# Kernel tuning notes

Hardware: AMD Instinct MI355X
Metric: run time of the kernel (lower is better)

The kernel has to match this reference:

```python
import jax, jax.numpy as jnp
import numpy as np

B, Q, D, E, V, K = 128, 32, 512, 300, 50000, 21

def kernel_mus(n):
    mus = [1.0]
    if n == 1:
        return mus
    bin_size = 2.0 / (n - 1)
    mus.append(1 - bin_size / 2)
    for i in range(1, n - 1):
        mus.append(mus[i] - bin_size)
    return mus

def kernel_sigmas(n):
    if n == 1:
        return [0.001]
    return [0.001] + [0.1] * (n - 1)

MU = jnp.asarray(kernel_mus(K), dtype=jnp.float32)        # (K,)
SIGMA = jnp.asarray(kernel_sigmas(K), dtype=jnp.float32)  # (K,)

def setup_inputs() -> dict:
    key = jax.random.key(0)
    k1, k2, k3, k4, k5, k6, k7 = jax.random.split(key, 7)
    query_idx = jax.random.randint(k1, (B, Q), 0, V)
    doc_idx = jax.random.randint(k2, (B, D), 0, V)
    query_len = jax.random.randint(k3, (B,), 1, Q + 1)
    doc_len = jax.random.randint(k4, (B,), 1, D + 1)
    emb_table = jax.random.normal(k5, (V, E), dtype=jnp.float32) * 0.1
    dense_w = jax.random.normal(k6, (1, K), dtype=jnp.float32) * 0.1
    dense_b = jax.random.normal(k7, (1,), dtype=jnp.float32) * 0.1
    return {"query_idx": query_idx, "doc_idx": doc_idx,
            "query_len": query_len, "doc_len": doc_len,
            "emb_table": emb_table, "dense_w": dense_w, "dense_b": dense_b}

def _l2norm(x):
    # F.normalize(x, p=2, dim=2): x / max(||x||, 1e-12)
    n = jnp.sqrt(jnp.sum(x * x, axis=-1, keepdims=True))
    return x / jnp.maximum(n, 1e-12)

def reference(query_idx, doc_idx, query_len, doc_len, emb_table, dense_w, dense_b):
    q_embed = _l2norm(emb_table[query_idx])   # (B,Q,E)
    d_embed = _l2norm(emb_table[doc_idx])     # (B,D,E)
    mask_q = (jnp.arange(Q)[None, :] < query_len[:, None]).astype(jnp.float32)  # (B,Q)
    mask_d = (jnp.arange(D)[None, :] < doc_len[:, None]).astype(jnp.float32)    # (B,D)
    sim = jnp.einsum('bqe,bde->bqd', q_embed, d_embed)  # (B,Q,D)
    # Gaussian kernel pooling: (B,Q,D,K) broadcast
    diff = sim[..., None] - MU
    pooling = jnp.exp(-(diff * diff) / (2.0 * SIGMA * SIGMA)) * mask_d[:, None, :, None]
    pooling_sum = jnp.sum(pooling, axis=2)                      # (B,Q,K)
    log_pool = jnp.log(jnp.clip(pooling_sum, 1e-10)) * mask_q[..., None] * 0.01
    log_pooling_sum = jnp.sum(log_pool, axis=1)                 # (B,K)
    score = jnp.squeeze(log_pooling_sum @ dense_w.T + dense_b, axis=1)  # (B,)
    return (score, log_pooling_sum)
```

## Files before the change

### kernel.cpp

```cpp
#include <hip/hip_runtime.h>

#define Bn 128
#define Qn 32
#define Dn 512
#define En 300
#define Kn 21
#define NC 16
#define CH 32
#define NKT 10
#define LDE 40
#define TILE_SH (CH * LDE)
#define SIMLD 36
#define NTHR 256
#define QK (Qn * Kn)

typedef __attribute__((ext_vector_type(8))) short bf16x8;
typedef __attribute__((ext_vector_type(4))) float f32x4;

#define SMEM_BYTES 51456

__device__ __forceinline__ float dot4(float4 a, float4 b) {
    return a.x * b.x + a.y * b.y + a.z * b.z + a.w * b.w;
}

#define ISSUE(arr, tok)                                                        \
    _Pragma("unroll")                                                          \
    for (int j2 = 0; j2 < NKT; ++j2) {                                         \
        const int k = j2 * 32 + il * 4;                                        \
        float4 v = {0.f, 0.f, 0.f, 0.f};                                       \
        if (k <= 296 && (tok) >= 0)                                            \
            v = *(const float4*)(table + (size_t)(tok) * En + k);              \
        arr[j2] = v;                                                           \
    }

#define COMMIT(arr, dst)                                                       \
    {                                                                          \
        float ss = 0.f;                                                        \
        _Pragma("unroll")                                                      \
        for (int j2 = 0; j2 < NKT; ++j2) ss += dot4(arr[j2], arr[j2]);         \
        ss += __shfl_xor(ss, 1);                                               \
        ss += __shfl_xor(ss, 2);                                               \
        ss += __shfl_xor(ss, 4);                                               \
        const float inv = 1.0f / fmaxf(sqrtf(ss), 1e-12f);                     \
        _Pragma("unroll")                                                      \
        for (int j2 = 0; j2 < NKT; ++j2) {                                     \
            const unsigned ax = __float_as_uint(arr[j2].x * inv) + 0x8000u;    \
            const unsigned ay = __float_as_uint(arr[j2].y * inv) + 0x8000u;    \
            const unsigned az = __float_as_uint(arr[j2].z * inv) + 0x8000u;    \
            const unsigned aw = __float_as_uint(arr[j2].w * inv) + 0x8000u;    \
            uint2 p;                                                           \
            p.x = __builtin_amdgcn_perm(ay, ax, 0x07060302u);                  \
            p.y = __builtin_amdgcn_perm(aw, az, 0x07060302u);                  \
            *(uint2*)&(dst)[j2 * TILE_SH + row * LDE + il * 4] = p;            \
        }                                                                      \
    }

__global__ __launch_bounds__(NTHR, 3)
void knrm_main(const int* __restrict__ qidx, const int* __restrict__ didx,
               const int* __restrict__ dlen_arr, const float* __restrict__ table,
               float* __restrict__ partial)
{
    const int g = blockIdx.x;
    const int idx2 = (g & 7) * 256 + (g >> 3);
    const int b = idx2 >> 4;
    const int c = idx2 & 15;
    const int dlen = dlen_arr[b];
    if (c * CH >= dlen) return;

    const int t = threadIdx.x;

    __shared__ __align__(16) char smem[SMEM_BYTES];
    short* dbuf = (short*)smem;
    short* qbuf = (short*)(smem + 25600);
    float* sim  = (float*)(smem + 25600);
    int*   idxb = (int*)(smem + 51200);

    if (t < CH) {
        const int doc = c * CH + t;
        idxb[t] = (doc < dlen) ? didx[b * Dn + doc] : -1;
    } else if (t < CH + Qn) {
        idxb[t] = qidx[b * Qn + (t - CH)];
    }
    __syncthreads();

    const int row = t >> 3;
    const int il  = t & 7;

    float4 lq[NKT], ldd[NKT];
    const int qtok = idxb[CH + row];
    const int dtok = idxb[row];
    ISSUE(lq, qtok)
    ISSUE(ldd, dtok)
    COMMIT(lq, qbuf)
    COMMIT(ldd, dbuf)
    __syncthreads();

    const int lane = t & 63;
    const int w = t >> 6;
    const int qt = w >> 1;
    const int dt = w & 1;
    const int frow = lane & 15;
    const int koct = lane >> 4;

    bf16x8 af[NKT];
    #pragma unroll
    for (int kt = 0; kt < NKT; ++kt)
        af[kt] = *(const bf16x8*)&qbuf[kt * TILE_SH + (qt * 16 + frow) * LDE + koct * 8];
    __syncthreads();

    f32x4 accS = {0.f, 0.f, 0.f, 0.f};
    #pragma unroll
    for (int kt = 0; kt < NKT; ++kt) {
        bf16x8 bf = *(const bf16x8*)&dbuf[kt * TILE_SH + (dt * 16 + frow) * LDE + koct * 8];
        accS = __builtin_amdgcn_mfma_f32_16x16x32_bf16(af[kt], bf, accS, 0, 0, 0);
    }
    #pragma unroll
    for (int r = 0; r < 4; ++r)
        sim[(qt * 16 + koct * 4 + r) * SIMLD + dt * 16 + frow] = accS[r];
    __syncthreads();

    const int pq = t >> 3;
    const int kg = t & 7;
    if (kg < 7) {
        float mu[3], cf[3];
        #pragma unroll
        for (int kk = 0; kk < 3; ++kk) {
            const int k = kg * 3 + kk;
            mu[kk] = (k == 0) ? 1.0f : 1.05f - 0.1f * (float)k;
            cf[kk] = (k == 0) ? -500000.0f : -50.0f;
        }
        float acc[3] = {0.f, 0.f, 0.f};
        const int cbase = c * CH;
        #pragma unroll
        for (int f4 = 0; f4 < 8; ++f4) {
            const float4 sv = *(const float4*)&sim[pq * SIMLD + f4 * 4];
            #pragma unroll
            for (int e = 0; e < 4; ++e) {
                const float se = (e == 0) ? sv.x : (e == 1) ? sv.y : (e == 2) ? sv.z : sv.w;
                const float s = (cbase + f4 * 4 + e < dlen) ? se : 1.0e3f;
                #pragma unroll
                for (int kk = 0; kk < 3; ++kk) {
                    const float d = s - mu[kk];
                    acc[kk] += __expf(cf[kk] * d * d);
                }
            }
        }
        float* pb = partial + (size_t)(b * NC + c) * QK + pq * Kn + kg * 3;
        pb[0] = acc[0]; pb[1] = acc[1]; pb[2] = acc[2];
    }
}

__global__ __launch_bounds__(704)
void knrm_reduce(const int* __restrict__ qlen_arr, const int* __restrict__ dlen_arr,
                 const float* __restrict__ partial, const float* __restrict__ dense_w,
                 const float* __restrict__ dense_b, float* __restrict__ out)
{
    __shared__ float sq[QK];
    __shared__ float lk[Kn];
    const int b = blockIdx.x;
    const int t = threadIdx.x;
    const int qlen = qlen_arr[b];
    const int ncu = min((dlen_arr[b] + CH - 1) >> 5, NC);
    if (t < QK) {
        const int q = t / Kn;
        float s = 0.f;
        for (int c = 0; c < ncu; ++c)
            s += partial[(size_t)(b * NC + c) * QK + t];
        sq[t] = (q < qlen) ? 0.01f * logf(fmaxf(s, 1e-10f)) : 0.f;
    }
    __syncthreads();
    if (t < Kn) {
        float l = 0.f;
        #pragma unroll
        for (int q = 0; q < Qn; ++q) l += sq[q * Kn + t];
        out[Bn + (size_t)b * Kn + t] = l;
        lk[t] = l;
    }
    __syncthreads();
    if (t == 0) {
        float sc = dense_b[0];
        #pragma unroll
        for (int k = 0; k < Kn; ++k) sc += lk[k] * dense_w[k];
        out[b] = sc;
    }
}

extern "C" void kernel_launch(void* const* d_in, const int* in_sizes, int n_in,
                              void* d_out, int out_size, void* d_ws, size_t ws_size,
                              hipStream_t stream)
{
    const int*   qidx  = (const int*)d_in[0];
    const int*   didx  = (const int*)d_in[1];
    const int*   qlen  = (const int*)d_in[2];
    const int*   dlen  = (const int*)d_in[3];
    const float* table = (const float*)d_in[4];
    const float* dw    = (const float*)d_in[5];
    const float* db    = (const float*)d_in[6];
    float* out     = (float*)d_out;
    float* partial = (float*)d_ws;

    knrm_main<<<dim3(Bn * NC), dim3(NTHR), 0, stream>>>(qidx, didx, dlen, table, partial);
    knrm_reduce<<<dim3(Bn), dim3(704), 0, stream>>>(qlen, dlen, partial, dw, db, out);
}
```

Before: 27.75 us.

## Load query fragments directly to registers and defer L2 normalization to sim

Query embeddings are now loaded by each wave straight into MFMA A-fragment registers, which removes the query shared-memory staging and the index-staging pass along with their barriers. Doc rows are stored unnormalized in bf16 with an XOR-swizzled row layout to avoid bank conflicts. The inverse norms are applied to the similarity output afterwards. Shared memory roughly halves, which can raise occupancy. The trade-off is that each query row is now loaded redundantly by both dt waves, and bf16 rounding now happens before normalization.

```diff
diff --git a/kernel.cpp b/kernel.cpp
--- a/kernel.cpp
+++ b/kernel.cpp
@@ -8,8 +8,7 @@
 #define NC 16
 #define CH 32
 #define NKT 10
-#define LDE 40
-#define TILE_SH (CH * LDE)
+#define ROWB 640
 #define SIMLD 36
 #define NTHR 256
 #define QK (Qn * Kn)
@@ -17,43 +16,30 @@
 typedef __attribute__((ext_vector_type(8))) short bf16x8;
 typedef __attribute__((ext_vector_type(4))) float f32x4;
 
-#define SMEM_BYTES 51456
+#define SIM_OFF  20480
+#define INVD_OFF 25088
+#define INVQ_OFF 25216
+#define SMEM_BYTES 25344
+
+#define SWZ(r, byte) ((byte) ^ (((r) & 7) << 4))
 
 __device__ __forceinline__ float dot4(float4 a, float4 b) {
     return a.x * b.x + a.y * b.y + a.z * b.z + a.w * b.w;
 }
 
-#define ISSUE(arr, tok)                                                        \
-    _Pragma("unroll")                                                          \
-    for (int j2 = 0; j2 < NKT; ++j2) {                                         \
-        const int k = j2 * 32 + il * 4;                                        \
-        float4 v = {0.f, 0.f, 0.f, 0.f};                                       \
-        if (k <= 296 && (tok) >= 0)                                            \
-            v = *(const float4*)(table + (size_t)(tok) * En + k);              \
-        arr[j2] = v;                                                           \
-    }
-
-#define COMMIT(arr, dst)                                                       \
-    {                                                                          \
-        float ss = 0.f;                                                        \
-        _Pragma("unroll")                                                      \
-        for (int j2 = 0; j2 < NKT; ++j2) ss += dot4(arr[j2], arr[j2]);         \
-        ss += __shfl_xor(ss, 1);                                               \
-        ss += __shfl_xor(ss, 2);                                               \
-        ss += __shfl_xor(ss, 4);                                               \
-        const float inv = 1.0f / fmaxf(sqrtf(ss), 1e-12f);                     \
-        _Pragma("unroll")                                                      \
-        for (int j2 = 0; j2 < NKT; ++j2) {                                     \
-            const unsigned ax = __float_as_uint(arr[j2].x * inv) + 0x8000u;    \
-            const unsigned ay = __float_as_uint(arr[j2].y * inv) + 0x8000u;    \
-            const unsigned az = __float_as_uint(arr[j2].z * inv) + 0x8000u;    \
-            const unsigned aw = __float_as_uint(arr[j2].w * inv) + 0x8000u;    \
-            uint2 p;                                                           \
-            p.x = __builtin_amdgcn_perm(ay, ax, 0x07060302u);                  \
-            p.y = __builtin_amdgcn_perm(aw, az, 0x07060302u);                  \
-            *(uint2*)&(dst)[j2 * TILE_SH + row * LDE + il * 4] = p;            \
-        }                                                                      \
-    }
+__device__ __forceinline__ bf16x8 pack8r(float4 lo, float4 hi) {
+    uint4 u;
+    u.x = __builtin_amdgcn_perm(__float_as_uint(lo.y) + 0x8000u,
+                                __float_as_uint(lo.x) + 0x8000u, 0x07060302u);
+    u.y = __builtin_amdgcn_perm(__float_as_uint(lo.w) + 0x8000u,
+                                __float_as_uint(lo.z) + 0x8000u, 0x07060302u);
+    u.z = __builtin_amdgcn_perm(__float_as_uint(hi.y) + 0x8000u,
+                                __float_as_uint(hi.x) + 0x8000u, 0x07060302u);
+    u.w = __builtin_amdgcn_perm(__float_as_uint(hi.w) + 0x8000u,
+                                __float_as_uint(hi.z) + 0x8000u, 0x07060302u);
+    union { uint4 u4; bf16x8 v; } cv; cv.u4 = u;
+    return cv.v;
+}
 
 __global__ __launch_bounds__(NTHR, 3)
 void knrm_main(const int* __restrict__ qidx, const int* __restrict__ didx,
@@ -68,55 +54,84 @@
     if (c * CH >= dlen) return;
 
     const int t = threadIdx.x;
-
-    __shared__ __align__(16) char smem[SMEM_BYTES];
-    short* dbuf = (short*)smem;
-    short* qbuf = (short*)(smem + 25600);
-    float* sim  = (float*)(smem + 25600);
-    int*   idxb = (int*)(smem + 51200);
-
-    if (t < CH) {
-        const int doc = c * CH + t;
-        idxb[t] = (doc < dlen) ? didx[b * Dn + doc] : -1;
-    } else if (t < CH + Qn) {
-        idxb[t] = qidx[b * Qn + (t - CH)];
-    }
-    __syncthreads();
-
-    const int row = t >> 3;
-    const int il  = t & 7;
-
-    float4 lq[NKT], ldd[NKT];
-    const int qtok = idxb[CH + row];
-    const int dtok = idxb[row];
-    ISSUE(lq, qtok)
-    ISSUE(ldd, dtok)
-    COMMIT(lq, qbuf)
-    COMMIT(ldd, dbuf)
-    __syncthreads();
-
     const int lane = t & 63;
     const int w = t >> 6;
     const int qt = w >> 1;
     const int dt = w & 1;
     const int frow = lane & 15;
     const int koct = lane >> 4;
-
+    const int row = t >> 3;
+    const int il  = t & 7;
+
+    __shared__ __align__(16) char smem[SMEM_BYTES];
+    char*  dbuf = smem;
+    float* sim  = (float*)(smem + SIM_OFF);
+    float* invd = (float*)(smem + INVD_OFF);
+    float* invq = (float*)(smem + INVQ_OFF);
+
+    const int qrow_i = qt * 16 + frow;
+    const int qtok = qidx[b * Qn + qrow_i];
+    const int dstage = c * CH + row;
+    const int dtok = (dstage < dlen) ? didx[b * Dn + dstage] : -1;
+    const float* qrow = table + (size_t)qtok * En;
+    const float* drow = table + (size_t)dtok * En;
+    const float4 z4 = make_float4(0.f, 0.f, 0.f, 0.f);
+
+    float4 ldd[10];
+    #pragma unroll
+    for (int i = 0; i < 5; ++i) {
+        const int f0 = (il + 8 * i) * 8;
+        ldd[2*i]   = (f0     <= 296 && dtok >= 0) ? *(const float4*)(drow + f0)     : z4;
+        ldd[2*i+1] = (f0 + 4 <= 296 && dtok >= 0) ? *(const float4*)(drow + f0 + 4) : z4;
+    }
+    float4 lq[20];
+    #pragma unroll
+    for (int kt = 0; kt < NKT; ++kt) {
+        const int f0 = kt * 32 + koct * 8;
+        lq[2*kt]   = (f0     <= 296) ? *(const float4*)(qrow + f0)     : z4;
+        lq[2*kt+1] = (f0 + 4 <= 296) ? *(const float4*)(qrow + f0 + 4) : z4;
+    }
+
+    float ssd = 0.f;
+    #pragma unroll
+    for (int i = 0; i < 10; ++i) ssd += dot4(ldd[i], ldd[i]);
+    #pragma unroll
+    for (int i = 0; i < 5; ++i) {
+        const int slot = il + 8 * i;
+        const bf16x8 p = pack8r(ldd[2*i], ldd[2*i+1]);
+        *(bf16x8*)(dbuf + SWZ(row, row * ROWB + slot * 16)) = p;
+    }
+    ssd += __shfl_xor(ssd, 1);
+    ssd += __shfl_xor(ssd, 2);
+    ssd += __shfl_xor(ssd, 4);
+    if (il == 0) invd[row] = 1.0f / fmaxf(sqrtf(ssd), 1e-12f);
+
+    float ssq = 0.f;
     bf16x8 af[NKT];
     #pragma unroll
-    for (int kt = 0; kt < NKT; ++kt)
-        af[kt] = *(const bf16x8*)&qbuf[kt * TILE_SH + (qt * 16 + frow) * LDE + koct * 8];
-    __syncthreads();
-
+    for (int kt = 0; kt < NKT; ++kt) {
+        ssq += dot4(lq[2*kt], lq[2*kt]) + dot4(lq[2*kt+1], lq[2*kt+1]);
+        af[kt] = pack8r(lq[2*kt], lq[2*kt+1]);
+    }
+    ssq += __shfl_xor(ssq, 16);
+    ssq += __shfl_xor(ssq, 32);
+    if (dt == 0 && koct == 0) invq[qrow_i] = 1.0f / fmaxf(sqrtf(ssq), 1e-12f);
+
+    __syncthreads();
+
+    const int dr = dt * 16 + frow;
     f32x4 accS = {0.f, 0.f, 0.f, 0.f};
     #pragma unroll
     for (int kt = 0; kt < NKT; ++kt) {
-        bf16x8 bf = *(const bf16x8*)&dbuf[kt * TILE_SH + (dt * 16 + frow) * LDE + koct * 8];
+        const bf16x8 bf = *(const bf16x8*)(dbuf + SWZ(dr, dr * ROWB + kt * 64 + koct * 16));
         accS = __builtin_amdgcn_mfma_f32_16x16x32_bf16(af[kt], bf, accS, 0, 0, 0);
     }
-    #pragma unroll
-    for (int r = 0; r < 4; ++r)
-        sim[(qt * 16 + koct * 4 + r) * SIMLD + dt * 16 + frow] = accS[r];
+    const float idd = invd[dr];
+    #pragma unroll
+    for (int r = 0; r < 4; ++r) {
+        const int q = qt * 16 + koct * 4 + r;
+        sim[q * SIMLD + dr] = accS[r] * invq[q] * idd;
+    }
     __syncthreads();
 
     const int pq = t >> 3;
```

After: 39.37 us. +41.9%, slower.

## Replace per-kernel exp with geometric recurrence over evenly spaced Gaussian means

Applied to the files above, without the earlier changes.

The Gaussian pooling is rewritten so each thread takes 4 similarity values and computes all 20 wide kernels using two exps and a running multiplication by exp(-10|s|). It exploits the even spacing of the kernel means, and the constant factor exp(-50 mu^2) is moved into the reduce kernel. Partial sums are combined across the 8 lanes of each row with shuffles before being written. This removes about 3x more exp calls than before and makes all lanes active. The cost is possible overflow or underflow in the recurrence (large starting x multiplied by small factors), plus the shuffle reductions.

```diff
diff --git a/kernel.cpp b/kernel.cpp
--- a/kernel.cpp
+++ b/kernel.cpp
@@ -120,33 +120,47 @@
     __syncthreads();
 
     const int pq = t >> 3;
-    const int kg = t & 7;
-    if (kg < 7) {
-        float mu[3], cf[3];
+    const int dl = t & 7;
+    const int cbase = c * CH + dl * 4;
+    const float4 sv = *(const float4*)&sim[pq * SIMLD + dl * 4];
+
+    float acc[Kn];
+    #pragma unroll
+    for (int k = 0; k < Kn; ++k) acc[k] = 0.f;
+
+    float sarr[4];
+    sarr[0] = (cbase + 0 < dlen) ? sv.x : 1.0e3f;
+    sarr[1] = (cbase + 1 < dlen) ? sv.y : 1.0e3f;
+    sarr[2] = (cbase + 2 < dlen) ? sv.z : 1.0e3f;
+    sarr[3] = (cbase + 3 < dlen) ? sv.w : 1.0e3f;
+
+    #pragma unroll
+    for (int j = 0; j < 4; ++j) {
+        const float sj = sarr[j];
+        const float sm1 = sj - 1.0f;
+        acc[0] += __expf(-500000.f * sm1 * sm1);
+        const float sa = fabsf(sj);
+        float x = __expf((105.f - 50.f * sa) * sa);
+        const float rr = __expf(-10.f * sa);
+        if (sj >= 0.f) {
+            #pragma unroll
+            for (int k = 1; k <= 20; ++k) { x *= rr; acc[k] += x; }
+        } else {
+            #pragma unroll
+            for (int k = 1; k <= 20; ++k) { x *= rr; acc[21 - k] += x; }
+        }
+    }
+
+    #pragma unroll
+    for (int k = 0; k < Kn; ++k) {
+        acc[k] += __shfl_xor(acc[k], 1);
+        acc[k] += __shfl_xor(acc[k], 2);
+        acc[k] += __shfl_xor(acc[k], 4);
+    }
+    if (dl == 0) {
+        float* pb = partial + (size_t)(b * NC + c) * QK + pq * Kn;
         #pragma unroll
-        for (int kk = 0; kk < 3; ++kk) {
-            const int k = kg * 3 + kk;
-            mu[kk] = (k == 0) ? 1.0f : 1.05f - 0.1f * (float)k;
-            cf[kk] = (k == 0) ? -500000.0f : -50.0f;
-        }
-        float acc[3] = {0.f, 0.f, 0.f};
-        const int cbase = c * CH;
-        #pragma unroll
-        for (int f4 = 0; f4 < 8; ++f4) {
-            const float4 sv = *(const float4*)&sim[pq * SIMLD + f4 * 4];
-            #pragma unroll
-            for (int e = 0; e < 4; ++e) {
-                const float se = (e == 0) ? sv.x : (e == 1) ? sv.y : (e == 2) ? sv.z : sv.w;
-                const float s = (cbase + f4 * 4 + e < dlen) ? se : 1.0e3f;
-                #pragma unroll
-                for (int kk = 0; kk < 3; ++kk) {
-                    const float d = s - mu[kk];
-                    acc[kk] += __expf(cf[kk] * d * d);
-                }
-            }
-        }
-        float* pb = partial + (size_t)(b * NC + c) * QK + pq * Kn + kg * 3;
-        pb[0] = acc[0]; pb[1] = acc[1]; pb[2] = acc[2];
+        for (int k = 0; k < Kn; ++k) pb[k] = acc[k];
     }
 }
 
@@ -163,9 +177,14 @@
     const int ncu = min((dlen_arr[b] + CH - 1) >> 5, NC);
     if (t < QK) {
         const int q = t / Kn;
+        const int k = t - q * Kn;
         float s = 0.f;
         for (int c = 0; c < ncu; ++c)
             s += partial[(size_t)(b * NC + c) * QK + t];
+        if (k > 0) {
+            const float mk = 1.05f - 0.1f * (float)k;
+            s *= __expf(-50.f * mk * mk);
+        }
         sq[t] = (q < qlen) ? 0.01f * logf(fmaxf(s, 1e-10f)) : 0.f;
     }
     __syncthreads();
```

Measured after the change: 29.29 us. +5.5%, slower.

## Fuse main and reduce kernels into one 1024-thread block per batch

Applied to the files above, without the earlier changes.

Replaces the 2048-block gather/pool kernel plus separate reduce kernel with a single kernel of one 1024-thread block per batch element. Each block loops over 128-doc chunks, prefetching the next chunk's embeddings while computing MFMA similarities and Gaussian pooling, then reduces partials in shared memory and computes log-sum and score in place. This removes the second launch and the global partial-buffer traffic. In exchange it cuts the grid to 128 blocks on a GPU with many more CUs, and serialises up to four chunks per block.

```diff
diff --git a/kernel.cpp b/kernel.cpp
--- a/kernel.cpp
+++ b/kernel.cpp
@@ -5,19 +5,21 @@
 #define Dn 512
 #define En 300
 #define Kn 21
-#define NC 16
-#define CH 32
+#define DR 128
+#define NRMAX 4
 #define NKT 10
 #define LDE 40
-#define TILE_SH (CH * LDE)
+#define QTILE (Qn * LDE)
+#define DTILE (DR * LDE)
 #define SIMLD 36
-#define NTHR 256
-#define QK (Qn * Kn)
+#define NTHR 1024
 
 typedef __attribute__((ext_vector_type(8))) short bf16x8;
 typedef __attribute__((ext_vector_type(4))) float f32x4;
 
-#define SMEM_BYTES 51456
+#define QBUF_OFF 102400
+#define SIM_OFF  128000
+#define SMEM_BYTES 146432
 
 __device__ __forceinline__ float dot4(float4 a, float4 b) {
     return a.x * b.x + a.y * b.y + a.z * b.z + a.w * b.w;
@@ -33,7 +35,7 @@
         arr[j2] = v;                                                           \
     }
 
-#define COMMIT(arr, dst)                                                       \
+#define COMMIT(arr, dst, TS)                                                   \
     {                                                                          \
         float ss = 0.f;                                                        \
         _Pragma("unroll")                                                      \
@@ -51,121 +53,120 @@
             uint2 p;                                                           \
             p.x = __builtin_amdgcn_perm(ay, ax, 0x07060302u);                  \
             p.y = __builtin_amdgcn_perm(aw, az, 0x07060302u);                  \
-            *(uint2*)&(dst)[j2 * TILE_SH + row * LDE + il * 4] = p;            \
+            *(uint2*)&(dst)[j2 * (TS) + row * LDE + il * 4] = p;               \
         }                                                                      \
     }
 
-__global__ __launch_bounds__(NTHR, 3)
-void knrm_main(const int* __restrict__ qidx, const int* __restrict__ didx,
-               const int* __restrict__ dlen_arr, const float* __restrict__ table,
-               float* __restrict__ partial)
+__global__ __launch_bounds__(NTHR, 1)
+void knrm_fused(const int* __restrict__ qidx, const int* __restrict__ didx,
+                const int* __restrict__ qlen_arr, const int* __restrict__ dlen_arr,
+                const float* __restrict__ table, const float* __restrict__ dense_w,
+                const float* __restrict__ dense_b, float* __restrict__ out)
 {
-    const int g = blockIdx.x;
-    const int idx2 = (g & 7) * 256 + (g >> 3);
-    const int b = idx2 >> 4;
-    const int c = idx2 & 15;
+    const int b = blockIdx.x;
     const int dlen = dlen_arr[b];
-    if (c * CH >= dlen) return;
-
+    const int qlen = qlen_arr[b];
     const int t = threadIdx.x;
 
     __shared__ __align__(16) char smem[SMEM_BYTES];
     short* dbuf = (short*)smem;
-    short* qbuf = (short*)(smem + 25600);
-    float* sim  = (float*)(smem + 25600);
-    int*   idxb = (int*)(smem + 51200);
-
-    if (t < CH) {
-        const int doc = c * CH + t;
-        idxb[t] = (doc < dlen) ? didx[b * Dn + doc] : -1;
-    } else if (t < CH + Qn) {
-        idxb[t] = qidx[b * Qn + (t - CH)];
-    }
-    __syncthreads();
-
+    short* qbuf = (short*)(smem + QBUF_OFF);
+    float* simb = (float*)(smem + SIM_OFF);
+    float* pool = (float*)smem;
+    float* sq   = (float*)(smem + 10752);
+    float* lk   = (float*)(smem + 13440);
+
+    const int lane = t & 63;
+    const int w  = t >> 6;
+    const int gg = w >> 2;
+    const int wq = w & 3;
+    const int qt = wq >> 1;
+    const int dt = wq & 1;
+    const int frow = lane & 15;
+    const int koct = lane >> 4;
     const int row = t >> 3;
     const int il  = t & 7;
 
-    float4 lq[NKT], ldd[NKT];
-    const int qtok = idxb[CH + row];
-    const int dtok = idxb[row];
-    ISSUE(lq, qtok)
-    ISSUE(ldd, dtok)
-    COMMIT(lq, qbuf)
-    COMMIT(ldd, dbuf)
-    __syncthreads();
-
-    const int lane = t & 63;
-    const int w = t >> 6;
-    const int qt = w >> 1;
-    const int dt = w & 1;
-    const int frow = lane & 15;
-    const int koct = lane >> 4;
+    float4 ld[NKT];
+    int dtok = (row < dlen) ? didx[b * Dn + row] : -1;
+    ISSUE(ld, dtok)
+    if (t < 256) {
+        float4 lq[NKT];
+        const int qtok = qidx[b * Qn + row];
+        ISSUE(lq, qtok)
+        COMMIT(lq, qbuf, QTILE)
+    }
+    COMMIT(ld, dbuf, DTILE)
+    __syncthreads();
 
     bf16x8 af[NKT];
     #pragma unroll
     for (int kt = 0; kt < NKT; ++kt)
-        af[kt] = *(const bf16x8*)&qbuf[kt * TILE_SH + (qt * 16 + frow) * LDE + koct * 8];
-    __syncthreads();
-
-    f32x4 accS = {0.f, 0.f, 0.f, 0.f};
+        af[kt] = *(const bf16x8*)&qbuf[kt * QTILE + (qt * 16 + frow) * LDE + koct * 8];
+
+    const int u  = t & 255;
+    const int pq = u >> 3;
+    const int kg = u & 7;
+    float mu[3], cf[3];
     #pragma unroll
-    for (int kt = 0; kt < NKT; ++kt) {
-        bf16x8 bf = *(const bf16x8*)&dbuf[kt * TILE_SH + (dt * 16 + frow) * LDE + koct * 8];
-        accS = __builtin_amdgcn_mfma_f32_16x16x32_bf16(af[kt], bf, accS, 0, 0, 0);
-    }
-    #pragma unroll
-    for (int r = 0; r < 4; ++r)
-        sim[(qt * 16 + koct * 4 + r) * SIMLD + dt * 16 + frow] = accS[r];
-    __syncthreads();
-
-    const int pq = t >> 3;
-    const int kg = t & 7;
-    if (kg < 7) {
-        float mu[3], cf[3];
-        #pragma unroll
-        for (int kk = 0; kk < 3; ++kk) {
-            const int k = kg * 3 + kk;
-            mu[kk] = (k == 0) ? 1.0f : 1.05f - 0.1f * (float)k;
-            cf[kk] = (k == 0) ? -500000.0f : -50.0f;
+    for (int kk = 0; kk < 3; ++kk) {
+        const int k = kg * 3 + kk;
+        mu[kk] = (k == 0) ? 1.0f : 1.05f - 0.1f * (float)k;
+        cf[kk] = (k == 0) ? -500000.0f : -50.0f;
+    }
+    float acc[3] = {0.f, 0.f, 0.f};
+
+    const int nr = min((dlen + DR - 1) >> 7, NRMAX);
+    for (int it = 0; it < nr; ++it) {
+        const bool more = (it + 1 < nr);
+        if (more) {
+            const int d1 = (it + 1) * DR + row;
+            dtok = (d1 < dlen) ? didx[b * Dn + d1] : -1;
+            ISSUE(ld, dtok)
         }
-        float acc[3] = {0.f, 0.f, 0.f};
-        const int cbase = c * CH;
-        #pragma unroll
-        for (int f4 = 0; f4 < 8; ++f4) {
-            const float4 sv = *(const float4*)&sim[pq * SIMLD + f4 * 4];
+
+        f32x4 accS = {0.f, 0.f, 0.f, 0.f};
+        #pragma unroll
+        for (int kt = 0; kt < NKT; ++kt) {
+            const bf16x8 bf = *(const bf16x8*)
+                &dbuf[kt * DTILE + (gg * 32 + dt * 16 + frow) * LDE + koct * 8];
+            accS = __builtin_amdgcn_mfma_f32_16x16x32_bf16(af[kt], bf, accS, 0, 0, 0);
+        }
+        #pragma unroll
+        for (int r = 0; r < 4; ++r)
+            simb[gg * (Qn * SIMLD) + (qt * 16 + koct * 4 + r) * SIMLD + dt * 16 + frow] = accS[r];
+        __syncthreads();
+
+        if (more) COMMIT(ld, dbuf, DTILE)
+
+        if (kg < 7) {
+            const int docg = it * DR + gg * 32;
             #pragma unroll
-            for (int e = 0; e < 4; ++e) {
-                const float se = (e == 0) ? sv.x : (e == 1) ? sv.y : (e == 2) ? sv.z : sv.w;
-                const float s = (cbase + f4 * 4 + e < dlen) ? se : 1.0e3f;
+            for (int f4 = 0; f4 < 8; ++f4) {
+                const float4 sv = *(const float4*)&simb[gg * (Qn * SIMLD) + pq * SIMLD + f4 * 4];
                 #pragma unroll
-                for (int kk = 0; kk < 3; ++kk) {
-                    const float d = s - mu[kk];
-                    acc[kk] += __expf(cf[kk] * d * d);
+                for (int e = 0; e < 4; ++e) {
+                    const float se = (e == 0) ? sv.x : (e == 1) ? sv.y : (e == 2) ? sv.z : sv.w;
+                    const float s = (docg + f4 * 4 + e < dlen) ? se : 1.0e3f;
+                    #pragma unroll
+                    for (int kk = 0; kk < 3; ++kk) {
+                        const float d = s - mu[kk];
+                        acc[kk] += __expf(cf[kk] * d * d);
+                    }
                 }
             }
         }
-        float* pb = partial + (size_t)(b * NC + c) * QK + pq * Kn + kg * 3;
+        __syncthreads();
+    }
+
+    if (kg < 7) {
+        float* pb = pool + gg * 672 + pq * Kn + kg * 3;
         pb[0] = acc[0]; pb[1] = acc[1]; pb[2] = acc[2];
     }
-}
-
-__global__ __launch_bounds__(704)
-void knrm_reduce(const int* __restrict__ qlen_arr, const int* __restrict__ dlen_arr,
-                 const float* __restrict__ partial, const float* __restrict__ dense_w,
-                 const float* __restrict__ dense_b, float* __restrict__ out)
-{
-    __shared__ float sq[QK];
-    __shared__ float lk[Kn];
-    const int b = blockIdx.x;
-    const int t = threadIdx.x;
-    const int qlen = qlen_arr[b];
-    const int ncu = min((dlen_arr[b] + CH - 1) >> 5, NC);
-    if (t < QK) {
+    __syncthreads();
+    if (t < Qn * Kn) {
         const int q = t / Kn;
-        float s = 0.f;
-        for (int c = 0; c < ncu; ++c)
-            s += partial[(size_t)(b * NC + c) * QK + t];
+        const float s = pool[t] + pool[672 + t] + pool[1344 + t] + pool[2016 + t];
         sq[t] = (q < qlen) ? 0.01f * logf(fmaxf(s, 1e-10f)) : 0.f;
     }
     __syncthreads();
@@ -196,9 +197,7 @@
     const float* table = (const float*)d_in[4];
     const float* dw    = (const float*)d_in[5];
     const float* db    = (const float*)d_in[6];
-    float* out     = (float*)d_out;
-    float* partial = (float*)d_ws;
-
-    knrm_main<<<dim3(Bn * NC), dim3(NTHR), 0, stream>>>(qidx, didx, dlen, table, partial);
-    knrm_reduce<<<dim3(Bn), dim3(704), 0, stream>>>(qlen, dlen, partial, dw, db, out);
+    float* out = (float*)d_out;
+
+    knrm_fused<<<dim3(Bn), dim3(NTHR), 0, stream>>>(qidx, didx, qlen, dlen, table, dw, db, out);
 }
```

Measured after the change: 41.88 us. +50.9%, slower.
